# Kernel tuning notes

Measured on AMD Instinct MI355X. Metric: run time of the kernel, lower is better.

Reference implementation:

```python
import jax, jax.numpy as jnp
import numpy as np

B, L, D, H, K_DELAYS = 8, 2048, 512, 8, 8
DH = D // H


def setup_inputs() -> dict:
    key = jax.random.key(0)
    ks = jax.random.split(key, 6)
    def lin_w(k):
        return 0.02 * jax.random.normal(k, (D, D), jnp.float32)
    return {
        "x_q":  jax.random.normal(ks[0], (B, L, D), jnp.float32),
        "x_kv": jax.random.normal(ks[1], (B, L, D), jnp.float32),
        "Wq": lin_w(ks[2]), "bq": jnp.zeros((D,), jnp.float32),
        "Wk": lin_w(ks[3]), "bk": jnp.zeros((D,), jnp.float32),
        "Wv": lin_w(ks[4]), "bv": jnp.zeros((D,), jnp.float32),
        "Wo": lin_w(ks[5]), "bo": jnp.zeros((D,), jnp.float32),
    }


def reference(x_q, x_kv, Wq, bq, Wk, bk, Wv, bv, Wo, bo):
    Bx, Lx, Dx = x_q.shape

    def proj(x, W, b):  # torch Linear: x @ W.T + b, then split heads -> [B,H,L,dh]
        return (x @ W.T + b).reshape(Bx, Lx, H, DH).transpose(0, 2, 1, 3)

    q = proj(x_q, Wq, bq)
    k = proj(x_kv, Wk, bk)
    v = proj(x_kv, Wv, bv)

    # FFT-based autocorrelation over the time axis (axis=2)
    qz = q - q.mean(axis=2, keepdims=True)
    kz = k - k.mean(axis=2, keepdims=True)
    Qf = jnp.fft.rfft(qz, axis=2)
    Kf = jnp.fft.rfft(kz, axis=2)
    corr = jnp.fft.irfft(Qf * jnp.conj(Kf), n=Lx, axis=2).mean(axis=-1)  # [B,H,L]
    # torch expands corr to [B,H,Lq,Lk] then means over Lq -> identical to corr
    score = corr

    K = min(K_DELAYS, Lx)
    vals, idx = jax.lax.top_k(score, K)                    # [B,H,K]
    w = vals / (vals.sum(axis=-1, keepdims=True) + 1e-12)
    w = jax.lax.stop_gradient(w)                           # .detach() in torch

    # circular shift by -delay == gather at (t + delay) mod L
    t = jnp.arange(Lx)
    pos = (t[None, None, None, :] + idx[..., None]) % Lx   # [B,H,K,L]
    v_sh = jnp.take_along_axis(v[:, :, None, :, :], pos[..., None], axis=3)  # [B,H,K,L,dh]
    out = jnp.einsum('bhk,bhkld->bhld', w, v_sh)           # weighted sum over delays

    out = out.transpose(0, 2, 1, 3).reshape(Bx, Lx, Dx)
    return out @ Wo.T + bo
```

## Files before the change

kernel.cpp:

```cpp
#include <hip/hip_runtime.h>
#include <math.h>

#define BB 8
#define LL 2048
#define DD 512
#define HH 8
#define DHH 64
#define KD 8
#define MM (BB*LL)

typedef _Float16 f16x2 __attribute__((ext_vector_type(2)));
typedef _Float16 f16x4 __attribute__((ext_vector_type(4)));
typedef _Float16 f16x8 __attribute__((ext_vector_type(8)));
typedef float    f32x4 __attribute__((ext_vector_type(4)));

__device__ inline void cvt8(const float* __restrict__ s, _Float16* hp, _Float16* lp) {
    const float4 a = *(const float4*)s;
    const float4 b = *(const float4*)(s + 4);
    const float v[8] = {a.x, a.y, a.z, a.w, b.x, b.y, b.z, b.w};
    f16x8 hi, lo;
#pragma unroll
    for (int j = 0; j < 8; j++) {
        const _Float16 h = (_Float16)v[j];
        hi[j] = h;
        lo[j] = (_Float16)((v[j] - (float)h) * 512.0f);
    }
    *(f16x8*)hp = hi;
    if (lp) *(f16x8*)lp = lo;
}

__global__ __launch_bounds__(256) void prep_all(const float* __restrict__ xq,
                                                const float* __restrict__ xkv,
                                                const float* __restrict__ Wq, const float* __restrict__ Wk,
                                                const float* __restrict__ Wv, const float* __restrict__ Wo,
                                                _Float16* __restrict__ Xq_h, _Float16* __restrict__ Xq_l,
                                                _Float16* __restrict__ Xkv_h, _Float16* __restrict__ Xkv_l,
                                                _Float16* __restrict__ Wq_h, _Float16* __restrict__ Wq_l,
                                                _Float16* __restrict__ Wk_h, _Float16* __restrict__ Wk_l,
                                                _Float16* __restrict__ Wv_h, _Float16* __restrict__ Wo_h) {
    const int bid = blockIdx.x;
    if (bid < 8192) {
        const int g = bid * 256 + threadIdx.x;
        const int which = g >> 20;
        const size_t idx = (size_t)(g & 1048575) * 8;
        const float* src = which ? xkv : xq;
        _Float16* dh = which ? Xkv_h : Xq_h;
        _Float16* dl = which ? Xkv_l : Xq_l;
        cvt8(src + idx, dh + idx, dl + idx);
    } else {
        const int g = (bid - 8192) * 256 + threadIdx.x;
        const int which = g >> 15;
        const size_t idx = (size_t)(g & 32767) * 8;
        if (which == 0)      cvt8(Wq + idx, Wq_h + idx, Wq_l + idx);
        else if (which == 1) cvt8(Wk + idx, Wk_h + idx, Wk_l + idx);
        else if (which == 2) cvt8(Wv + idx, Wv_h + idx, nullptr);
        else                 cvt8(Wo + idx, Wo_h + idx, nullptr);
    }
}

__device__ __forceinline__ void stage16(const _Float16* g, const _Float16* l) {
    __builtin_amdgcn_global_load_lds(
        (const __attribute__((address_space(1))) void*)g,
        (__attribute__((address_space(3))) void*)l,
        16, 0, 0);
}

template<int NPROD, int MODE>
__device__ __forceinline__ void gemm_body(const _Float16* __restrict__ Ag,
                                          const _Float16* __restrict__ Al_g,
                                          const _Float16* __restrict__ Bg,
                                          const _Float16* __restrict__ Bl_g,
                                          const float* __restrict__ bias,
                                          void* __restrict__ Cv,
                                          _Float16* lds, int l0) {
    _Float16* Ah = lds;
    _Float16* Bh = lds + 4096;
    _Float16* Al = (NPROD == 3) ? lds + 8192  : lds;
    _Float16* Bl = (NPROD == 3) ? lds + 12288 : lds;

    const int t  = threadIdx.x;
    const int m0 = (((l0 >> 5) << 3) | (l0 & 7)) * 128;
    const int n0 = ((l0 >> 3) & 3) * 128;

    const int wv   = t >> 6;
    const int lane = t & 63;
    const int wm   = (wv >> 1) * 64;
    const int wn   = (wv & 1) * 64;
    const int lm   = lane & 15;
    const int quad = lane >> 4;

    int srow[2], schk[2], sgrp[2];
#pragma unroll
    for (int i = 0; i < 2; i++) {
        const int s = (i * 4 + wv) * 64 + lane;
        srow[i] = s >> 2;
        schk[i] = (s & 3) ^ ((srow[i] >> 1) & 3);
        sgrp[i] = (i * 4 + wv) * 512;
    }

    f32x4 acc0[4][4] = {};
    f32x4 acc1[4][4] = {};

#define ASWZ(R, q) ((size_t)(R) * 32 + (size_t)((((q) ^ (((R) >> 1) & 3))) * 8))

    for (int k0 = 0; k0 < 512; k0 += 32) {
        __syncthreads();
#pragma unroll
        for (int i = 0; i < 2; i++) {
            const size_t offA = (size_t)(m0 + srow[i]) * 512 + k0 + schk[i] * 8;
            const size_t offB = (size_t)(n0 + srow[i]) * 512 + k0 + schk[i] * 8;
            stage16(Ag + offA, Ah + sgrp[i]);
            stage16(Bg + offB, Bh + sgrp[i]);
            if (NPROD == 3) {
                stage16(Al_g + offA, Al + sgrp[i]);
                stage16(Bl_g + offB, Bl + sgrp[i]);
            }
        }
        __syncthreads();

        f16x8 afh[4], bf[4];
#pragma unroll
        for (int mt = 0; mt < 4; mt++)
            afh[mt] = *(f16x8*)&Ah[ASWZ(wm + mt * 16 + lm, quad)];
#pragma unroll
        for (int nt = 0; nt < 4; nt++)
            bf[nt] = *(f16x8*)&Bh[ASWZ(wn + nt * 16 + lm, quad)];

#pragma unroll
        for (int mt = 0; mt < 4; mt++)
#pragma unroll
            for (int nt = 0; nt < 4; nt++)
                acc0[mt][nt] = __builtin_amdgcn_mfma_f32_16x16x32_f16(afh[mt], bf[nt], acc0[mt][nt], 0, 0, 0);

        if (NPROD == 3) {
            f16x8 afl[4];
#pragma unroll
            for (int mt = 0; mt < 4; mt++)
                afl[mt] = *(f16x8*)&Al[ASWZ(wm + mt * 16 + lm, quad)];
#pragma unroll
            for (int mt = 0; mt < 4; mt++)
#pragma unroll
                for (int nt = 0; nt < 4; nt++)
                    acc1[mt][nt] = __builtin_amdgcn_mfma_f32_16x16x32_f16(afl[mt], bf[nt], acc1[mt][nt], 0, 0, 0);
#pragma unroll
            for (int nt = 0; nt < 4; nt++)
                bf[nt] = *(f16x8*)&Bl[ASWZ(wn + nt * 16 + lm, quad)];
#pragma unroll
            for (int mt = 0; mt < 4; mt++)
#pragma unroll
                for (int nt = 0; nt < 4; nt++)
                    acc1[mt][nt] = __builtin_amdgcn_mfma_f32_16x16x32_f16(afh[mt], bf[nt], acc1[mt][nt], 0, 0, 0);
        }
    }
#undef ASWZ

#pragma unroll
    for (int mt = 0; mt < 4; mt++) {
#pragma unroll
        for (int nt = 0; nt < 4; nt++) {
            const int n = n0 + wn + nt * 16 + lm;
            const float bv = bias[n];
            float val[4];
#pragma unroll
            for (int r = 0; r < 4; r++) {
                val[r] = acc0[mt][nt][r] + bv;
                if (NPROD == 3) val[r] += acc1[mt][nt][r] * (1.0f / 512.0f);
            }
            const int mbase = m0 + wm + mt * 16 + quad * 4;
            const int b_idx = mbase >> 11;
            const int lbase = mbase & 2047;
            if (MODE == 0) {
                float* C = (float*)Cv;
#pragma unroll
                for (int r = 0; r < 4; r++) C[(size_t)(mbase + r) * 512 + n] = val[r];
            } else if (MODE == 1) {
                float* C = (float*)Cv;
                float4 pv = make_float4(val[0], val[1], val[2], val[3]);
                *(float4*)&C[((size_t)(b_idx * 512 + n)) * 2048 + lbase] = pv;
            } else {
                _Float16* C = (_Float16*)Cv;
#pragma unroll
                for (int r = 0; r < 4; r++)
                    C[(size_t)b_idx * 1048576 + (size_t)(n >> 6) * 131072
                      + (size_t)(lbase + r) * 64 + (n & 63)] = (_Float16)val[r];
            }
        }
    }
}

__global__ __launch_bounds__(256, 2) void gemm_qk(const _Float16* __restrict__ A0h, const _Float16* __restrict__ A0l,
                                                  const _Float16* __restrict__ B0h, const _Float16* __restrict__ B0l,
                                                  const float* __restrict__ bias0, float* __restrict__ C0,
                                                  const _Float16* __restrict__ A1h, const _Float16* __restrict__ A1l,
                                                  const _Float16* __restrict__ B1h, const _Float16* __restrict__ B1l,
                                                  const float* __restrict__ bias1, float* __restrict__ C1) {
    __shared__ __align__(16) _Float16 lds[16384];
    const int prob = blockIdx.x >> 9;
    const int l0   = blockIdx.x & 511;
    if (prob == 0)
        gemm_body<3, 1>(A0h, A0l, B0h, B0l, bias0, C0, lds, l0);
    else
        gemm_body<3, 1>(A1h, A1l, B1h, B1l, bias1, C1, lds, l0);
}

__global__ __launch_bounds__(256, 2) void gemm_o(const _Float16* __restrict__ Ah_g,
                                                 const _Float16* __restrict__ Bh_g,
                                                 const float* __restrict__ bias,
                                                 float* __restrict__ C) {
    __shared__ __align__(16) _Float16 lds[8192];
    gemm_body<1, 0>(Ah_g, Ah_g, Bh_g, Bh_g, bias, C, lds, blockIdx.x);
}

#define PAD3(i) ((i) + ((i) >> 3))

__device__ inline float2 cmul2(float2 a, float2 w) {
    return make_float2(a.x * w.x - a.y * w.y, a.x * w.y + a.y * w.x);
}
__device__ inline float2 cadd2(float2 a, float2 b) { return make_float2(a.x + b.x, a.y + b.y); }
__device__ inline float2 csub2(float2 a, float2 b) { return make_float2(a.x - b.x, a.y - b.y); }

__global__ __launch_bounds__(256) void fft_fwd(const float* __restrict__ qT,
                                               const float* __restrict__ kT,
                                               float* __restrict__ specP) {
    const int blk  = blockIdx.x;
    const int bh   = blk >> 4;
    const int part = blk & 15;
    const int t    = threadIdx.x;
    __shared__ float2 Zs[2304];
    __shared__ float2 Wt[1024];

#pragma unroll
    for (int s = 0; s < 4; s++) {
        const int j = t + s * 256;
        float sv, cv;
        __sincosf(2.0f * (float)M_PI * (float)j / 2048.0f, &sv, &cv);
        Wt[j] = make_float2(cv, -sv);
    }

    float2 pacc[8];
#pragma unroll
    for (int s = 0; s < 8; s++) pacc[s] = make_float2(0.0f, 0.0f);

    const int low5 = t & 31, hi3 = t >> 5;
    const int low2 = t & 3,  hi6 = t >> 2;

    for (int j4 = 0; j4 < 4; j4++) {
        const int seq = bh * 64 + part * 4 + j4;
        const float* qp = qT + (size_t)seq * 2048;
        const float* kp = kT + (size_t)seq * 2048;
        float2 z[8];
#pragma unroll
        for (int s = 0; s < 8; s++) z[s] = make_float2(qp[t + 256 * s], kp[t + 256 * s]);
        __syncthreads();

#pragma unroll
        for (int sp = 0; sp < 4; sp++) {
            float2 u = z[sp], v = z[sp + 4];
            z[sp]     = cadd2(u, v);
            z[sp + 4] = cmul2(csub2(u, v), Wt[t + 256 * sp]);
        }
#pragma unroll
        for (int base = 0; base < 8; base += 4)
#pragma unroll
            for (int q2 = 0; q2 < 2; q2++) {
                float2 u = z[base + q2], v = z[base + q2 + 2];
                z[base + q2]     = cadd2(u, v);
                z[base + q2 + 2] = cmul2(csub2(u, v), Wt[2 * (t + 256 * q2)]);
            }
        {
            const float2 w = Wt[4 * t];
#pragma unroll
            for (int e = 0; e < 8; e += 2) {
                float2 u = z[e], v = z[e + 1];
                z[e]     = cadd2(u, v);
                z[e + 1] = cmul2(csub2(u, v), w);
            }
        }

#pragma unroll
        for (int s = 0; s < 8; s++) Zs[PAD3(t + 256 * s)] = z[s];
        __syncthreads();
#pragma unroll
        for (int s = 0; s < 8; s++) z[s] = Zs[PAD3(low5 + 32 * s + 256 * hi3)];

#pragma unroll
        for (int sp = 0; sp < 4; sp++) {
            float2 u = z[sp], v = z[sp + 4];
            z[sp]     = cadd2(u, v);
            z[sp + 4] = cmul2(csub2(u, v), Wt[8 * (low5 + 32 * sp)]);
        }
#pragma unroll
        for (int base = 0; base < 8; base += 4)
#pragma unroll
            for (int q2 = 0; q2 < 2; q2++) {
                float2 u = z[base + q2], v = z[base + q2 + 2];
                z[base + q2]     = cadd2(u, v);
                z[base + q2 + 2] = cmul2(csub2(u, v), Wt[16 * (low5 + 32 * q2)]);
            }
        {
            const float2 w = Wt[32 * low5];
#pragma unroll
            for (int e = 0; e < 8; e += 2) {
                float2 u = z[e], v = z[e + 1];
                z[e]     = cadd2(u, v);
                z[e + 1] = cmul2(csub2(u, v), w);
            }
        }

#pragma unroll
        for (int s = 0; s < 8; s++) Zs[PAD3(low5 + 32 * s + 256 * hi3)] = z[s];
        __syncthreads();
#pragma unroll
        for (int s = 0; s < 8; s++) z[s] = Zs[PAD3(low2 + 4 * s + 32 * hi6)];

#pragma unroll
        for (int sp = 0; sp < 4; sp++) {
            float2 u = z[sp], v = z[sp + 4];
            z[sp]     = cadd2(u, v);
            z[sp + 4] = cmul2(csub2(u, v), Wt[64 * (low2 + 4 * sp)]);
        }
#pragma unroll
        for (int base = 0; base < 8; base += 4)
#pragma unroll
            for (int q2 = 0; q2 < 2; q2++) {
                float2 u = z[base + q2], v = z[base + q2 + 2];
                z[base + q2]     = cadd2(u, v);
                z[base + q2 + 2] = cmul2(csub2(u, v), Wt[128 * (low2 + 4 * q2)]);
            }
        {
            const float2 w = Wt[256 * low2];
#pragma unroll
            for (int e = 0; e < 8; e += 2) {
                float2 u = z[e], v = z[e + 1];
                z[e]     = cadd2(u, v);
                z[e + 1] = cmul2(csub2(u, v), w);
            }
        }

#pragma unroll
        for (int s = 0; s < 8; s++) Zs[PAD3(low2 + 4 * s + 32 * hi6)] = z[s];
        __syncthreads();
#pragma unroll
        for (int s = 0; s < 8; s++) z[s] = Zs[PAD3(8 * t + s)];

#pragma unroll
        for (int base = 0; base < 8; base += 4) {
            {
                float2 u = z[base], v = z[base + 2];
                z[base]     = cadd2(u, v);
                z[base + 2] = csub2(u, v);
            }
            {
                float2 u = z[base + 1], v = z[base + 3];
                float2 d = csub2(u, v);
                z[base + 1] = cadd2(u, v);
                z[base + 3] = make_float2(d.y, -d.x);
            }
        }
#pragma unroll
        for (int e = 0; e < 8; e += 2) {
            float2 u = z[e], v = z[e + 1];
            z[e]     = cadd2(u, v);
            z[e + 1] = csub2(u, v);
        }

#pragma unroll
        for (int s = 0; s < 8; s++) Zs[PAD3(8 * t + s)] = z[s];
        __syncthreads();

#pragma unroll
        for (int s = 0; s < 8; s++) {
            const int p  = t + 256 * s;
            const int f  = (int)(__brev((unsigned)p) >> 21);
            const int fm = (2048 - f) & 2047;
            const int p2 = (int)(__brev((unsigned)fm) >> 21);
            const float2 zf = Zs[PAD3(p)];
            const float2 zm = Zs[PAD3(p2)];
            const float qr = 0.5f * (zf.x + zm.x);
            const float qi = 0.5f * (zf.y - zm.y);
            const float kr = 0.5f * (zf.y + zm.y);
            const float ki = 0.5f * (zm.x - zf.x);
            if (f != 0) {
                pacc[s].x += qr * kr + qi * ki;
                pacc[s].y += qi * kr - qr * ki;
            }
        }
    }

    float2* outp = (float2*)specP + (size_t)blk * 2048;
#pragma unroll
    for (int s = 0; s < 8; s++) outp[t + 256 * s] = pacc[s];
}

__device__ inline void build_twiddle(float2* Wt, int tid, float sign) {
#pragma unroll
    for (int s = 0; s < 4; s++) {
        const int j = tid + s * 256;
        const float a = 2.0f * (float)M_PI * (float)j / 2048.0f;
        float sv, cv;
        __sincosf(a, &sv, &cv);
        Wt[j] = make_float2(cv, sign * sv);
    }
}

__device__ inline void fft2048_stages(float2* Z, const float2* Wt, int tid) {
    for (int st = 0; st < 11; st++) {
        const int half = 1 << st;
        const int shift = 10 - st;
#pragma unroll
        for (int r = 0; r < 4; r++) {
            const int m   = tid + r * 256;
            const int grp = m >> st;
            const int pos = m & (half - 1);
            const int i0  = (grp << (st + 1)) + pos;
            const int i1  = i0 + half;
            const float2 w = Wt[pos << shift];
            const float2 a = Z[i0];
            const float2 b = Z[i1];
            const float tr = b.x * w.x - b.y * w.y;
            const float ti = b.x * w.y + b.y * w.x;
            Z[i0] = make_float2(a.x + tr, a.y + ti);
            Z[i1] = make_float2(a.x - tr, a.y - ti);
        }
        __syncthreads();
    }
}

__global__ __launch_bounds__(256, 2) void gemm_v_fftinv(const _Float16* __restrict__ Ah_g,
                                                        const _Float16* __restrict__ Bh_g,
                                                        const float* __restrict__ bias,
                                                        _Float16* __restrict__ C,
                                                        const float* __restrict__ specP,
                                                        int* __restrict__ delays,
                                                        float* __restrict__ weights) {
    __shared__ __align__(16) char smem[24608];
    const int bid = blockIdx.x;
    const int tid = threadIdx.x;

    if (bid >= 64) {
        gemm_body<1, 2>(Ah_g, Ah_g, Bh_g, Bh_g, bias, C, (_Float16*)smem, bid - 64);
        return;
    }

    const int bh = bid;
    float2* Z  = (float2*)smem;
    float2* Wt = (float2*)(smem + 16384);
    float*  wv = (float*)(smem + 24576);
    int*    wi = (int*)(smem + 24592);

    build_twiddle(Wt, tid, +1.0f);

    const float2* sp = (const float2*)specP + (size_t)bh * 16 * 2048;
#pragma unroll
    for (int s = 0; s < 8; s++) {
        const int p = tid + s * 256;
        float2 acc = make_float2(0.0f, 0.0f);
#pragma unroll
        for (int part = 0; part < 16; part++) {
            const float2 v = sp[part * 2048 + p];
            acc.x += v.x; acc.y += v.y;
        }
        Z[p] = acc;
    }
    __syncthreads();
    fft2048_stages(Z, Wt, tid);

    const float scale = 1.0f / (2048.0f * 64.0f);
    float cv[8];
#pragma unroll
    for (int s = 0; s < 8; s++) cv[s] = Z[tid + s * 256].x * scale;

    float bkv[KD];
    int   bki[KD];
#pragma unroll
    for (int k = 0; k < KD; k++) {
        float lv = -1e30f;
        int   li = 1 << 30;
#pragma unroll
        for (int s = 0; s < 8; s++) {
            const int idx = tid + s * 256;
            if (cv[s] > lv || (cv[s] == lv && idx < li)) { lv = cv[s]; li = idx; }
        }
#pragma unroll
        for (int off = 1; off < 64; off <<= 1) {
            const float v2 = __shfl_xor(lv, off);
            const int   i2 = __shfl_xor(li, off);
            if (v2 > lv || (v2 == lv && i2 < li)) { lv = v2; li = i2; }
        }
        if ((tid & 63) == 0) { wv[tid >> 6] = lv; wi[tid >> 6] = li; }
        __syncthreads();
        float bv = wv[0];
        int   bi = wi[0];
#pragma unroll
        for (int j = 1; j < 4; j++) {
            const float v2 = wv[j];
            const int   i2 = wi[j];
            if (v2 > bv || (v2 == bv && i2 < bi)) { bv = v2; bi = i2; }
        }
        bkv[k] = bv;
        bki[k] = bi;
        if ((bi & 255) == tid) {
            const int slot = bi >> 8;
#pragma unroll
            for (int s = 0; s < 8; s++)
                if (s == slot) cv[s] = -1e30f;
        }
        __syncthreads();
    }

    if (tid == 0) {
        float sum = 0.0f;
#pragma unroll
        for (int k = 0; k < KD; k++) sum += bkv[k];
        const float inv = 1.0f / (sum + 1e-12f);
#pragma unroll
        for (int k = 0; k < KD; k++) {
            weights[bh * KD + k] = bkv[k] * inv;
            delays[bh * KD + k]  = bki[k];
        }
    }
}

__global__ __launch_bounds__(256) void gather_ws(const _Float16* __restrict__ v,
                                                 const int* __restrict__ delays,
                                                 const float* __restrict__ weights,
                                                 _Float16* __restrict__ outb) {
    const int gp = blockIdx.x * 256 + threadIdx.x;
    const int c8 = gp & 63;
    const int m  = gp >> 6;
    const int l  = m & 2047;
    const int b  = m >> 11;
    const int ch = c8 * 8;
    const int h  = ch >> 6;
    const int dh = ch & 63;
    const int bh = b * 8 + h;

    const _Float16* vb = v + (size_t)bh * 131072;
    float a[8] = {};
#pragma unroll
    for (int k = 0; k < KD; k++) {
        const int   d = delays[bh * KD + k];
        const float w = weights[bh * KD + k];
        const int   p = (l + d) & 2047;
        const f16x8 pv = *(const f16x8*)&vb[p * 64 + dh];
#pragma unroll
        for (int j = 0; j < 8; j++) a[j] = fmaf(w, (float)pv[j], a[j]);
    }
    f16x8 ov;
#pragma unroll
    for (int j = 0; j < 8; j++) ov[j] = (_Float16)a[j];
    *(f16x8*)&outb[(size_t)m * 512 + ch] = ov;
}

extern "C" void kernel_launch(void* const* d_in, const int* in_sizes, int n_in,
                              void* d_out, int out_size, void* d_ws, size_t ws_size,
                              hipStream_t stream) {
    const float* x_q  = (const float*)d_in[0];
    const float* x_kv = (const float*)d_in[1];
    const float* Wq   = (const float*)d_in[2];
    const float* bq   = (const float*)d_in[3];
    const float* Wk   = (const float*)d_in[4];
    const float* bk   = (const float*)d_in[5];
    const float* Wv   = (const float*)d_in[6];
    const float* bv   = (const float*)d_in[7];
    const float* Wo   = (const float*)d_in[8];
    const float* bo   = (const float*)d_in[9];
    float* out = (float*)d_out;

    char* ws = (char*)d_ws;
    _Float16* Xq_h  = (_Float16*)(ws + 0);
    _Float16* Xq_l  = (_Float16*)(ws + 16777216);
    _Float16* Xkv_h = (_Float16*)(ws + 33554432);
    _Float16* Xkv_l = (_Float16*)(ws + 50331648);
    _Float16* Wq_h  = (_Float16*)(ws + 67108864);
    _Float16* Wq_l  = (_Float16*)(ws + 67633152);
    _Float16* Wk_h  = (_Float16*)(ws + 68157440);
    _Float16* Wk_l  = (_Float16*)(ws + 68681728);
    _Float16* Wv_h  = (_Float16*)(ws + 69206016);
    _Float16* Wo_h  = (_Float16*)(ws + 69730304);
    int*      dely  = (int*)    (ws + 70254592);
    float*    wgt   = (float*)  (ws + 70256640);
    float*    specP = (float*)  (ws + 50331648);
    _Float16* vh    = (_Float16*)(ws + 0);
    _Float16* gbuf  = (_Float16*)(ws + 16777216);
    float*    qf32  = (float*)d_out;

    dim3 blk(256);

    prep_all<<<dim3(8704), blk, 0, stream>>>(x_q, x_kv, Wq, Wk, Wv, Wo,
                                             Xq_h, Xq_l, Xkv_h, Xkv_l,
                                             Wq_h, Wq_l, Wk_h, Wk_l, Wv_h, Wo_h);

    const size_t kOff  = 70258688;
    const bool   merged = ws_size >= kOff + 33554432;
    float* kf32 = merged ? (float*)(ws + kOff) : (float*)(ws + 0);

    if (merged) {
        gemm_qk<<<dim3(1024), blk, 0, stream>>>(Xq_h, Xq_l, Wq_h, Wq_l, bq, qf32,
                                                Xkv_h, Xkv_l, Wk_h, Wk_l, bk, kf32);
    } else {
        gemm_qk<<<dim3(512), blk, 0, stream>>>(Xq_h, Xq_l, Wq_h, Wq_l, bq, qf32,
                                               Xq_h, Xq_l, Wq_h, Wq_l, bq, qf32);
        gemm_qk<<<dim3(512), blk, 0, stream>>>(Xkv_h, Xkv_l, Wk_h, Wk_l, bk, kf32,
                                               Xkv_h, Xkv_l, Wk_h, Wk_l, bk, kf32);
    }

    fft_fwd<<<dim3(1024), blk, 0, stream>>>(qf32, kf32, specP);

    gemm_v_fftinv<<<dim3(576), blk, 0, stream>>>(Xkv_h, Wv_h, bv, vh, specP, dely, wgt);

    gather_ws<<<dim3(4096), blk, 0, stream>>>(vh, dely, wgt, gbuf);

    gemm_o<<<dim3(512), blk, 0, stream>>>(gbuf, Wo_h, bo, out);
}
```

Measured before the change: 277.1 us.

## Fuse delay-weighted gather into output projection GEMM and prefetch FFT inputs

Removes the standalone gather kernel and its fp16 intermediate buffer by computing the weighted circular-shift sum directly while staging the A tile of the output-projection GEMM. The forward FFT kernel now prefetches the next sequence's inputs into registers, and when workspace allows it uses twice as many blocks (32 parts per head) to raise parallelism. The workspace layout is rearranged to fit the larger partial-spectrum buffer. The trade-off is that each GEMM block now issues 8 scattered global loads per A element before the barrier, which is not pipelined with the MFMA work, and the inverse FFT must sum more partial spectra.

```diff
diff --git a/kernel.cpp b/kernel.cpp
--- a/kernel.cpp
+++ b/kernel.cpp
@@ -65,6 +65,8 @@
         16, 0, 0);
 }
 
+#define ASWZ(R, q) ((size_t)(R) * 32 + (size_t)((((q) ^ (((R) >> 1) & 3))) * 8))
+
 template<int NPROD, int MODE>
 __device__ __forceinline__ void gemm_body(const _Float16* __restrict__ Ag,
                                           const _Float16* __restrict__ Al_g,
@@ -101,8 +103,6 @@
     f32x4 acc0[4][4] = {};
     f32x4 acc1[4][4] = {};
 
-#define ASWZ(R, q) ((size_t)(R) * 32 + (size_t)((((q) ^ (((R) >> 1) & 3))) * 8))
-
     for (int k0 = 0; k0 < 512; k0 += 32) {
         __syncthreads();
 #pragma unroll
@@ -152,7 +152,6 @@
                     acc1[mt][nt] = __builtin_amdgcn_mfma_f32_16x16x32_f16(afh[mt], bf[nt], acc1[mt][nt], 0, 0, 0);
         }
     }
-#undef ASWZ
 
 #pragma unroll
     for (int mt = 0; mt < 4; mt++) {
@@ -169,11 +168,7 @@
             const int mbase = m0 + wm + mt * 16 + quad * 4;
             const int b_idx = mbase >> 11;
             const int lbase = mbase & 2047;
-            if (MODE == 0) {
-                float* C = (float*)Cv;
-#pragma unroll
-                for (int r = 0; r < 4; r++) C[(size_t)(mbase + r) * 512 + n] = val[r];
-            } else if (MODE == 1) {
+            if (MODE == 1) {
                 float* C = (float*)Cv;
                 float4 pv = make_float4(val[0], val[1], val[2], val[3]);
                 *(float4*)&C[((size_t)(b_idx * 512 + n)) * 2048 + lbase] = pv;
@@ -203,12 +198,106 @@
         gemm_body<3, 1>(A1h, A1l, B1h, B1l, bias1, C1, lds, l0);
 }
 
-__global__ __launch_bounds__(256, 2) void gemm_o(const _Float16* __restrict__ Ah_g,
-                                                 const _Float16* __restrict__ Bh_g,
-                                                 const float* __restrict__ bias,
-                                                 float* __restrict__ C) {
+__global__ __launch_bounds__(256, 2) void gemm_og(const _Float16* __restrict__ vh,
+                                                  const int* __restrict__ delays,
+                                                  const float* __restrict__ weights,
+                                                  const _Float16* __restrict__ Bg,
+                                                  const float* __restrict__ bias,
+                                                  float* __restrict__ C) {
     __shared__ __align__(16) _Float16 lds[8192];
-    gemm_body<1, 0>(Ah_g, Ah_g, Bh_g, Bh_g, bias, C, lds, blockIdx.x);
+    _Float16* Ah = lds;
+    _Float16* Bh = lds + 4096;
+
+    const int t  = threadIdx.x;
+    const int l0 = blockIdx.x;
+    const int m0 = (((l0 >> 5) << 3) | (l0 & 7)) * 128;
+    const int n0 = ((l0 >> 3) & 3) * 128;
+
+    const int wv   = t >> 6;
+    const int lane = t & 63;
+    const int wm   = (wv >> 1) * 64;
+    const int wn   = (wv & 1) * 64;
+    const int lm   = lane & 15;
+    const int quad = lane >> 4;
+
+    int srow[2], schk[2], sgrp[2];
+#pragma unroll
+    for (int i = 0; i < 2; i++) {
+        const int s = (i * 4 + wv) * 64 + lane;
+        srow[i] = s >> 2;
+        schk[i] = (s & 3) ^ ((srow[i] >> 1) & 3);
+        sgrp[i] = (i * 4 + wv) * 512;
+    }
+
+    const int bb  = m0 >> 11;
+    const int lml = m0 & 2047;
+
+    f32x4 acc0[4][4] = {};
+
+    for (int k0 = 0; k0 < 512; k0 += 32) {
+        const int h  = k0 >> 6;
+        const int bh = bb * 8 + h;
+        int   dj[KD];
+        float wj[KD];
+#pragma unroll
+        for (int j = 0; j < KD; j++) {
+            dj[j] = delays[bh * KD + j];
+            wj[j] = weights[bh * KD + j];
+        }
+
+        f16x8 ov[2];
+#pragma unroll
+        for (int i = 0; i < 2; i++) {
+            const int l  = lml + srow[i];
+            const int dh = (k0 & 63) + schk[i] * 8;
+            float a[8] = {};
+#pragma unroll
+            for (int j = 0; j < KD; j++) {
+                const int pos = (l + dj[j]) & 2047;
+                const f16x8 pv = *(const f16x8*)&vh[(size_t)bh * 131072 + pos * 64 + dh];
+#pragma unroll
+                for (int e = 0; e < 8; e++) a[e] = fmaf(wj[j], (float)pv[e], a[e]);
+            }
+#pragma unroll
+            for (int e = 0; e < 8; e++) ov[i][e] = (_Float16)a[e];
+        }
+
+        __syncthreads();
+#pragma unroll
+        for (int i = 0; i < 2; i++) {
+            *(f16x8*)&Ah[sgrp[i] + lane * 8] = ov[i];
+            const size_t offB = (size_t)(n0 + srow[i]) * 512 + k0 + schk[i] * 8;
+            stage16(Bg + offB, Bh + sgrp[i]);
+        }
+        __syncthreads();
+
+        f16x8 afh[4], bf[4];
+#pragma unroll
+        for (int mt = 0; mt < 4; mt++)
+            afh[mt] = *(f16x8*)&Ah[ASWZ(wm + mt * 16 + lm, quad)];
+#pragma unroll
+        for (int nt = 0; nt < 4; nt++)
+            bf[nt] = *(f16x8*)&Bh[ASWZ(wn + nt * 16 + lm, quad)];
+
+#pragma unroll
+        for (int mt = 0; mt < 4; mt++)
+#pragma unroll
+            for (int nt = 0; nt < 4; nt++)
+                acc0[mt][nt] = __builtin_amdgcn_mfma_f32_16x16x32_f16(afh[mt], bf[nt], acc0[mt][nt], 0, 0, 0);
+    }
+
+#pragma unroll
+    for (int mt = 0; mt < 4; mt++) {
+#pragma unroll
+        for (int nt = 0; nt < 4; nt++) {
+            const int n  = n0 + wn + nt * 16 + lm;
+            const float bv = bias[n];
+            const int mbase = m0 + wm + mt * 16 + quad * 4;
+#pragma unroll
+            for (int r = 0; r < 4; r++)
+                C[(size_t)(mbase + r) * 512 + n] = acc0[mt][nt][r] + bv;
+        }
+    }
 }
 
 #define PAD3(i) ((i) + ((i) >> 3))
@@ -221,10 +310,12 @@
 
 __global__ __launch_bounds__(256) void fft_fwd(const float* __restrict__ qT,
                                                const float* __restrict__ kT,
-                                               float* __restrict__ specP) {
+                                               float* __restrict__ specP,
+                                               int pshift) {
     const int blk  = blockIdx.x;
-    const int bh   = blk >> 4;
-    const int part = blk & 15;
+    const int bh   = blk >> pshift;
+    const int part = blk & ((1 << pshift) - 1);
+    const int JP   = 64 >> pshift;
     const int t    = threadIdx.x;
     __shared__ float2 Zs[2304];
     __shared__ float2 Wt[1024];
@@ -244,13 +335,26 @@
     const int low5 = t & 31, hi3 = t >> 5;
     const int low2 = t & 3,  hi6 = t >> 2;
 
-    for (int j4 = 0; j4 < 4; j4++) {
-        const int seq = bh * 64 + part * 4 + j4;
-        const float* qp = qT + (size_t)seq * 2048;
-        const float* kp = kT + (size_t)seq * 2048;
+    float2 zn[8];
+    {
+        const int seq0 = bh * 64 + part * JP;
+        const float* qp = qT + (size_t)seq0 * 2048;
+        const float* kp = kT + (size_t)seq0 * 2048;
+#pragma unroll
+        for (int s = 0; s < 8; s++) zn[s] = make_float2(qp[t + 256 * s], kp[t + 256 * s]);
+    }
+
+    for (int j4 = 0; j4 < JP; j4++) {
         float2 z[8];
 #pragma unroll
-        for (int s = 0; s < 8; s++) z[s] = make_float2(qp[t + 256 * s], kp[t + 256 * s]);
+        for (int s = 0; s < 8; s++) z[s] = zn[s];
+        if (j4 + 1 < JP) {
+            const int seq = bh * 64 + part * JP + j4 + 1;
+            const float* qp = qT + (size_t)seq * 2048;
+            const float* kp = kT + (size_t)seq * 2048;
+#pragma unroll
+            for (int s = 0; s < 8; s++) zn[s] = make_float2(qp[t + 256 * s], kp[t + 256 * s]);
+        }
         __syncthreads();
 
 #pragma unroll
@@ -432,7 +536,8 @@
                                                         _Float16* __restrict__ C,
                                                         const float* __restrict__ specP,
                                                         int* __restrict__ delays,
-                                                        float* __restrict__ weights) {
+                                                        float* __restrict__ weights,
+                                                        int nparts) {
     __shared__ __align__(16) char smem[24608];
     const int bid = blockIdx.x;
     const int tid = threadIdx.x;
@@ -445,19 +550,18 @@
     const int bh = bid;
     float2* Z  = (float2*)smem;
     float2* Wt = (float2*)(smem + 16384);
-    float*  wv = (float*)(smem + 24576);
-    int*    wi = (int*)(smem + 24592);
+    float*  wvs = (float*)(smem + 24576);
+    int*    wis = (int*)(smem + 24592);
 
     build_twiddle(Wt, tid, +1.0f);
 
-    const float2* sp = (const float2*)specP + (size_t)bh * 16 * 2048;
+    const float2* sp = (const float2*)specP + (size_t)bh * nparts * 2048;
 #pragma unroll
     for (int s = 0; s < 8; s++) {
         const int p = tid + s * 256;
         float2 acc = make_float2(0.0f, 0.0f);
-#pragma unroll
-        for (int part = 0; part < 16; part++) {
-            const float2 v = sp[part * 2048 + p];
+        for (int part = 0; part < nparts; part++) {
+            const float2 v = sp[(size_t)part * 2048 + p];
             acc.x += v.x; acc.y += v.y;
         }
         Z[p] = acc;
@@ -487,14 +591,14 @@
             const int   i2 = __shfl_xor(li, off);
             if (v2 > lv || (v2 == lv && i2 < li)) { lv = v2; li = i2; }
         }
-        if ((tid & 63) == 0) { wv[tid >> 6] = lv; wi[tid >> 6] = li; }
-        __syncthreads();
-        float bv = wv[0];
-        int   bi = wi[0];
+        if ((tid & 63) == 0) { wvs[tid >> 6] = lv; wis[tid >> 6] = li; }
+        __syncthreads();
+        float bv = wvs[0];
+        int   bi = wis[0];
 #pragma unroll
         for (int j = 1; j < 4; j++) {
-            const float v2 = wv[j];
-            const int   i2 = wi[j];
+            const float v2 = wvs[j];
+            const int   i2 = wis[j];
             if (v2 > bv || (v2 == bv && i2 < bi)) { bv = v2; bi = i2; }
         }
         bkv[k] = bv;
@@ -519,37 +623,6 @@
             delays[bh * KD + k]  = bki[k];
         }
     }
-}
-
-__global__ __launch_bounds__(256) void gather_ws(const _Float16* __restrict__ v,
-                                                 const int* __restrict__ delays,
-                                                 const float* __restrict__ weights,
-                                                 _Float16* __restrict__ outb) {
-    const int gp = blockIdx.x * 256 + threadIdx.x;
-    const int c8 = gp & 63;
-    const int m  = gp >> 6;
-    const int l  = m & 2047;
-    const int b  = m >> 11;
-    const int ch = c8 * 8;
-    const int h  = ch >> 6;
-    const int dh = ch & 63;
-    const int bh = b * 8 + h;
-
-    const _Float16* vb = v + (size_t)bh * 131072;
-    float a[8] = {};
-#pragma unroll
-    for (int k = 0; k < KD; k++) {
-        const int   d = delays[bh * KD + k];
-        const float w = weights[bh * KD + k];
-        const int   p = (l + d) & 2047;
-        const f16x8 pv = *(const f16x8*)&vb[p * 64 + dh];
-#pragma unroll
-        for (int j = 0; j < 8; j++) a[j] = fmaf(w, (float)pv[j], a[j]);
-    }
-    f16x8 ov;
-#pragma unroll
-    for (int j = 0; j < 8; j++) ov[j] = (_Float16)a[j];
-    *(f16x8*)&outb[(size_t)m * 512 + ch] = ov;
 }
 
 extern "C" void kernel_launch(void* const* d_in, const int* in_sizes, int n_in,
@@ -580,20 +653,21 @@
     _Float16* Wo_h  = (_Float16*)(ws + 69730304);
     int*      dely  = (int*)    (ws + 70254592);
     float*    wgt   = (float*)  (ws + 70256640);
-    float*    specP = (float*)  (ws + 50331648);
-    _Float16* vh    = (_Float16*)(ws + 0);
-    _Float16* gbuf  = (_Float16*)(ws + 16777216);
     float*    qf32  = (float*)d_out;
+
+    const size_t kOff   = 70258688;
+    const bool   merged = ws_size >= kOff + 33554432;
+
+    float*    kf32  = merged ? (float*)(ws + kOff)     : (float*)(ws + 0);
+    float*    specP = merged ? (float*)(ws + 0)        : (float*)(ws + 50331648);
+    _Float16* vh    = merged ? (_Float16*)(ws + 50331648) : (_Float16*)(ws + 0);
+    const int pshift = merged ? 5 : 4;
 
     dim3 blk(256);
 
     prep_all<<<dim3(8704), blk, 0, stream>>>(x_q, x_kv, Wq, Wk, Wv, Wo,
                                              Xq_h, Xq_l, Xkv_h, Xkv_l,
                                              Wq_h, Wq_l, Wk_h, Wk_l, Wv_h, Wo_h);
-
-    const size_t kOff  = 70258688;
-    const bool   merged = ws_size >= kOff + 33554432;
-    float* kf32 = merged ? (float*)(ws + kOff) : (float*)(ws + 0);
 
     if (merged) {
         gemm_qk<<<dim3(1024), blk, 0, stream>>>(Xq_h, Xq_l, Wq_h, Wq_l, bq, qf32,
@@ -605,11 +679,10 @@
                                                Xkv_h, Xkv_l, Wk_h, Wk_l, bk, kf32);
     }
 
-    fft_fwd<<<dim3(1024), blk, 0, stream>>>(qf32, kf32, specP);
-
-    gemm_v_fftinv<<<dim3(576), blk, 0, stream>>>(Xkv_h, Wv_h, bv, vh, specP, dely, wgt);
-
-    gather_ws<<<dim3(4096), blk, 0, stream>>>(vh, dely, wgt, gbuf);
-
-    gemm_o<<<dim3(512), blk, 0, stream>>>(gbuf, Wo_h, bo, out);
-}
+    fft_fwd<<<dim3(64 << pshift), blk, 0, stream>>>(qf32, kf32, specP, pshift);
+
+    gemm_v_fftinv<<<dim3(576), blk, 0, stream>>>(Xkv_h, Wv_h, bv, vh, specP, dely, wgt,
+                                                 1 << pshift);
+
+    gemm_og<<<dim3(512), blk, 0, stream>>>(vh, dely, wgt, Wo_h, bo, out);
+}
```

New measurement: 350.7 us. +26.5%, slower.
